# Optimization experiments

Measured on AMD Instinct MI355X. Metric: run time of the kernel, lower is better.

## Reference

```python
import jax, jax.numpy as jnp
import numpy as np

B, L, H, D, VOC, C, P = 16, 256, 6, 768, 32000, 20, 1
d = D // H
MAXF = 20
BN_EPS = 1e-5


def setup_inputs() -> dict:
    key = jax.random.key(0)
    ks = jax.random.split(key, 8)
    doc_tids = jax.random.randint(ks[0], (B, L), 0, VOC)
    TFs = jax.random.uniform(ks[1], (B, L), dtype=jnp.float32) * 20.0 + 1.0
    DFs = jax.random.uniform(ks[2], (B, L), dtype=jnp.float32) * 1000.0 + 1.0
    emb = jax.random.normal(ks[3], (VOC, D), dtype=jnp.float32) * 0.02
    fcW = jax.random.normal(ks[4], (C + P, D), dtype=jnp.float32) * 0.02
    fcb = jnp.zeros((C + P,), dtype=jnp.float32)
    weiW = jax.random.normal(ks[5], (2, H), dtype=jnp.float32) * 0.1
    weib = jnp.zeros((2,), dtype=jnp.float32)
    return dict(doc_tids=doc_tids, TFs=TFs, DFs=DFs, emb=emb,
                fcW=fcW, fcb=fcb, weiW=weiW, weib=weib)


def _bn(x):
    # BatchNorm over channel axis 1 (H), batch stats over all other axes (train mode, affine=False)
    m = x.mean(axis=(0, 2, 3), keepdims=True)
    v = x.var(axis=(0, 2, 3), keepdims=True)
    return (x - m) * jax.lax.rsqrt(v + BN_EPS)


def _leaky9(x):
    return jnp.where(x >= 0, x, 9.0 * x)


def reference(doc_tids, TFs, DFs, emb, fcW, fcb, weiW, weib):
    # --- EmbbedingTFIDF (eval mode, dropout off): tf-idf weighted embedding lookup ---
    tf = jnp.minimum(TFs, float(MAXF))
    idf = jnp.log1p(1.0 / DFs)
    x = emb[doc_tids] * (tf * idf)[:, :, None]          # (B, L, D)
    valid = doc_tids != 0
    # model flips pad_mask with logical_not, then co_weights[pad_mask] = 0
    invalid = ~(valid[:, :, None] & valid[:, None, :])  # (B, L, L) True -> zero out
    mask = invalid[:, None, :, :]                       # broadcast over heads

    def split_heads(h):
        return h.reshape(B, L, H, d).transpose(0, 2, 1, 3)  # (B, H, L, d)

    Q = split_heads(x)
    K = Q
    V = Q

    # --- nearAttention (layers=1) ---
    Vn = _bn(V)
    # DistMatrix: pairwise Euclidean distance dist[b,h,i,j] = ||K_i - Q_j||
    Ksq = jnp.sum(K * K, axis=-1)[..., :, None]
    Qsq = jnp.sum(Q * Q, axis=-1)[..., None, :]
    cross = jnp.einsum('bhid,bhjd->bhij', K, Q)
    co = jnp.sqrt(jnp.maximum(Ksq + Qsq - 2.0 * cross, 1e-12))  # (B, H, L, L)
    # BatchNorm1d(H) over flattened (B, H, L*L) == per-H stats over (0,2,3)
    co = _leaky9(_bn(co))
    co = jnp.where(mask, 0.0, co)
    co = jax.nn.softmax(co, axis=-1)
    co = jnp.where(jnp.isnan(co), 0.0, co)
    V_out = jnp.einsum('bhij,bhjd->bhid', co, Vn)
    Q_out = _bn(jnp.einsum('bhij,bhjd->bhid', co, Q))
    K_out = _bn(jnp.einsum('bhij,bhjd->bhid', co, K))

    # --- head ---
    Vc = V_out.transpose(0, 2, 1, 3).reshape(B, L, D)       # catHiddens
    V_lgts = jax.nn.softmax(Vc @ fcW.T + fcb, axis=-1)      # (B, L, C+P)
    cw = jnp.swapaxes(co, -1, -2).reshape(B, L * L, H)      # transpose then contiguous reshape
    cw = jax.nn.softmax(cw @ weiW.T + weib, axis=-1)        # (B, L*L, 2)
    cw = cw.reshape(B, L, L, 2).sum(axis=-2, keepdims=True)[:, :, :, 0]  # (B, L, 1)
    cw = jax.nn.softmax(cw, axis=-1)                        # softmax over singleton -> ones (faithful)
    logits = (cw * V_lgts).sum(axis=1)[:, :C]               # (B, C)
    logits = jax.nn.softmax(logits, axis=-1)
    return logits
```

## Files before the change

### kernel.cpp

```cpp
#include <hip/hip_runtime.h>
#include <hip/hip_bf16.h>
#include <math.h>

#define OFF_XH   0UL
#define OFF_XT   1572864UL
#define OFF_VC   3145728UL
#define OFF_SQ   4718592UL
#define OFF_PART 4767744UL
#define OFF_ACC  4780056UL
#define OFF_CTR  4780392UL
#define OFF_FCWB 4780396UL

typedef __attribute__((ext_vector_type(8))) __bf16 bf16x8;
typedef __attribute__((ext_vector_type(4))) float f32x4;
typedef __attribute__((ext_vector_type(8))) unsigned short u16x8;

__global__ __launch_bounds__(512) void k12_fused(const int* __restrict__ tids,
    const float* __restrict__ TF, const float* __restrict__ DF,
    const float* __restrict__ emb, unsigned short* __restrict__ xh,
    unsigned short* __restrict__ xT, float* __restrict__ sq,
    float* __restrict__ part, const float* __restrict__ fcW,
    unsigned short* __restrict__ fcWb, float* __restrict__ acc,
    unsigned int* __restrict__ ctr) {
  int bid = blockIdx.x;
  int xcd = bid & 7, idx = bid >> 3;
  int bh = xcd * 12 + idx % 12;
  int jq = idx / 12;
  int b = bh / 6, h = bh % 6;
  int tid = threadIdx.x;
  __shared__ unsigned short tile[32768];
  __shared__ float swd1[8], swd2[8], swv1[8], swv2[8];
  if (jq == 1) {
    if (tid < 168) {
      int i2 = bh * 168 + tid;
      fcWb[i2] = __bfloat16_as_ushort(__float2bfloat16(fcW[i2]));
    }
  } else if (jq == 0 && bh == 0) {
    if (tid < 336) acc[tid] = 0.0f;
    if (tid == 336) *ctr = 0u;
  }
  int sub = tid & 7, row0 = tid >> 3;
  int c16 = sub * 16;
  float ts1 = 0.0f, ts2 = 0.0f;
#pragma unroll
  for (int p = 0; p < 4; ++p) {
    int r = p * 64 + row0;
    int tok = b * 256 + r;
    int tv = tids[tok];
    float wgt = fminf(TF[tok], 20.0f) * log1pf(1.0f / DF[tok]);
    const float* er = emb + (size_t)tv * 768 + h * 128 + c16;
    float4 e0 = *(const float4*)er;
    float4 e1 = *(const float4*)(er + 4);
    float4 e2 = *(const float4*)(er + 8);
    float4 e3 = *(const float4*)(er + 12);
    float f[16] = {e0.x, e0.y, e0.z, e0.w, e1.x, e1.y, e1.z, e1.w,
                   e2.x, e2.y, e2.z, e2.w, e3.x, e3.y, e3.z, e3.w};
    u16x8 pk0, pk1;
    float s1 = 0.0f, s2 = 0.0f;
#pragma unroll
    for (int e = 0; e < 8; ++e) {
      __hip_bfloat16 hb = __float2bfloat16(f[e] * wgt);
      float g = __bfloat162float(hb);
      s1 += g; s2 += g * g;
      pk0[e] = __bfloat16_as_ushort(hb);
    }
#pragma unroll
    for (int e = 0; e < 8; ++e) {
      __hip_bfloat16 hb = __float2bfloat16(f[8 + e] * wgt);
      float g = __bfloat162float(hb);
      s1 += g; s2 += g * g;
      pk1[e] = __bfloat16_as_ushort(hb);
    }
    ts1 += s1; ts2 += s2;
    int rx = r & 7;
    *(u16x8*)&tile[r * 128 + (((sub * 2    ) ^ rx) * 8)] = pk0;
    *(u16x8*)&tile[r * 128 + (((sub * 2 + 1) ^ rx) * 8)] = pk1;
    if (jq == 0) {
      unsigned short* xo = xh + ((size_t)bh * 256 + r) * 128 + c16;
      *(u16x8*)xo = pk0;
      *(u16x8*)(xo + 8) = pk1;
    }
    s2 += __shfl_down(s2, 4); s2 += __shfl_down(s2, 2); s2 += __shfl_down(s2, 1);
    if (sub == 0)
      sq[(size_t)bh * 256 + r] = s2;
  }
  __syncthreads();
  if (jq == 3) {
    int ch = tid & 127, q = tid >> 7;
    int cc = ch >> 3, cs = ch & 7;
    unsigned int* xo = (unsigned int*)xT + ((size_t)bh * 128 + ch) * 128 + q * 32;
#pragma unroll
    for (int g = 0; g < 8; ++g) {
      unsigned int tmp[4];
#pragma unroll
      for (int k = 0; k < 4; ++k) {
        int t0 = q * 64 + (g * 4 + k) * 2;
        unsigned int lo = tile[ t0      * 128 + ((cc ^ ( t0      & 7)) * 8) + cs];
        unsigned int hi = tile[(t0 + 1) * 128 + ((cc ^ ((t0 + 1) & 7)) * 8) + cs];
        tmp[k] = lo | (hi << 16);
      }
      uint4 vv; vv.x = tmp[0]; vv.y = tmp[1]; vv.z = tmp[2]; vv.w = tmp[3];
      *(uint4*)(xo + g * 4) = vv;
    }
  }
  int w = tid >> 6, lane = tid & 63, quad = lane >> 4, l16 = lane & 15;
  const float* sqh = sq + (size_t)bh * 256;
  int it0 = w * 2;
  bf16x8 a2[2][4];
  float si2[2][4];
#pragma unroll
  for (int ith = 0; ith < 2; ++ith) {
    int ar = (it0 + ith) * 16 + l16, arx = ar & 7;
#pragma unroll
    for (int k0 = 0; k0 < 4; ++k0)
      a2[ith][k0] = *(const bf16x8*)&tile[ar * 128 + (((k0 * 4 + quad) ^ arx) * 8)];
#pragma unroll
    for (int r = 0; r < 4; ++r)
      si2[ith][r] = sqh[(it0 + ith) * 16 + quad * 4 + r];
  }
  float ls1 = 0.0f, ls2 = 0.0f;
#pragma unroll
  for (int jt = 0; jt < 4; ++jt) {
    int jr = jq * 64 + jt * 16 + l16, jrx = jr & 7;
    bf16x8 bfr[4];
#pragma unroll
    for (int k0 = 0; k0 < 4; ++k0)
      bfr[k0] = *(const bf16x8*)&tile[jr * 128 + (((k0 * 4 + quad) ^ jrx) * 8)];
    f32x4 acc0 = {0.0f, 0.0f, 0.0f, 0.0f}, acc1 = {0.0f, 0.0f, 0.0f, 0.0f};
#pragma unroll
    for (int k0 = 0; k0 < 4; ++k0) {
      acc0 = __builtin_amdgcn_mfma_f32_16x16x32_bf16(a2[0][k0], bfr[k0], acc0, 0, 0, 0);
      acc1 = __builtin_amdgcn_mfma_f32_16x16x32_bf16(a2[1][k0], bfr[k0], acc1, 0, 0, 0);
    }
    float sj = sqh[jr];
#pragma unroll
    for (int r = 0; r < 4; ++r) {
      float cv0 = sqrtf(fmaxf(si2[0][r] + sj - 2.0f * acc0[r], 1e-12f));
      float cv1 = sqrtf(fmaxf(si2[1][r] + sj - 2.0f * acc1[r], 1e-12f));
      ls1 += cv0 + cv1;
      ls2 += cv0 * cv0 + cv1 * cv1;
    }
  }
#pragma unroll
  for (int off = 32; off >= 1; off >>= 1) {
    ls1 += __shfl_down(ls1, off);
    ls2 += __shfl_down(ls2, off);
    ts1 += __shfl_down(ts1, off);
    ts2 += __shfl_down(ts2, off);
  }
  if (lane == 0) { swd1[w] = ls1; swd2[w] = ls2; swv1[w] = ts1; swv2[w] = ts2; }
  __syncthreads();
  if (tid == 0) {
    float d1 = 0.0f, d2 = 0.0f, v1 = 0.0f, v2 = 0.0f;
#pragma unroll
    for (int i = 0; i < 8; ++i) { d1 += swd1[i]; d2 += swd2[i]; v1 += swv1[i]; v2 += swv2[i]; }
    part[192 + (bh * 4 + jq) * 2 + 0] = d1;
    part[192 + (bh * 4 + jq) * 2 + 1] = d2;
    if (jq == 0) { part[bh * 2] = v1; part[bh * 2 + 1] = v2; }
  }
}

__global__ __launch_bounds__(256, 4) void k45_fused(const unsigned short* __restrict__ xh,
    const unsigned short* __restrict__ xT, const int* __restrict__ tids,
    const float* __restrict__ sq, const float* __restrict__ part,
    unsigned short* __restrict__ vc16) {
  int bid = blockIdx.x;
  int xcd = bid & 7, idx = bid >> 3;
  int bh = xcd * 12 + idx % 12;
  int p = idx / 12;
  int b = bh / 6, h = bh % 6;
  int tid = threadIdx.x, w = tid >> 6, lane = tid & 63;
  int quad = lane >> 4, l16 = lane & 15;
  int I = p * 16;
  __shared__ float svld[256];
  __shared__ float ssq[256];
  __shared__ unsigned short cot[16][264];
  __shared__ float smax[16][4];
  __shared__ float ssum[16][4];
  __shared__ float sstat[4];
  svld[tid] = (tids[b * 256 + tid] != 0) ? 1.0f : 0.0f;
  ssq[tid] = sq[(size_t)bh * 256 + tid];
  if (w == 0) {
    float c1 = 0.0f, c2 = 0.0f;
    {
      int bb = lane >> 2, jj = lane & 3;
      c1 = part[192 + ((bb * 6 + h) * 4 + jj) * 2 + 0];
      c2 = part[192 + ((bb * 6 + h) * 4 + jj) * 2 + 1];
    }
#pragma unroll
    for (int off = 32; off >= 1; off >>= 1) {
      c1 += __shfl_down(c1, off);
      c2 += __shfl_down(c2, off);
    }
    float v1 = 0.0f, v2 = 0.0f;
    if (lane < 16) {
      v1 = part[(lane * 6 + h) * 2 + 0];
      v2 = part[(lane * 6 + h) * 2 + 1];
    }
#pragma unroll
    for (int off = 8; off >= 1; off >>= 1) {
      v1 += __shfl_down(v1, off);
      v2 += __shfl_down(v2, off);
    }
    if (lane == 0) {
      float mean = c1 / 1048576.0f;
      float var = c2 / 1048576.0f - mean * mean;
      sstat[0] = mean;
      sstat[1] = rsqrtf(var + 1e-5f);
      float mv = v1 / 524288.0f;
      float vv = v2 / 524288.0f - mv * mv;
      sstat[2] = mv;
      sstat[3] = rsqrtf(vv + 1e-5f);
    }
  }
  const __bf16* xb = (const __bf16*)xh + (size_t)bh * 256 * 128;
  bf16x8 a[4];
#pragma unroll
  for (int k0 = 0; k0 < 4; ++k0)
    a[k0] = *(const bf16x8*)(xb + (size_t)(I + l16) * 128 + k0 * 32 + quad * 8);
  __syncthreads();
  float m = sstat[0], rsc = sstat[1];
  float rv[4], si[4];
#pragma unroll
  for (int r = 0; r < 4; ++r) {
    rv[r] = svld[I + quad * 4 + r];
    si[r] = ssq[I + quad * 4 + r];
  }
  float y[4][4];
#pragma unroll
  for (int tl = 0; tl < 4; ++tl) {
    int t = w * 4 + tl;
    f32x4 acc = {0.0f, 0.0f, 0.0f, 0.0f};
#pragma unroll
    for (int k0 = 0; k0 < 4; ++k0) {
      bf16x8 bfr = *(const bf16x8*)(xb + (size_t)(t * 16 + l16) * 128 + k0 * 32 + quad * 8);
      acc = __builtin_amdgcn_mfma_f32_16x16x32_bf16(a[k0], bfr, acc, 0, 0, 0);
    }
    float sj = ssq[t * 16 + l16];
    float cvld = svld[t * 16 + l16];
#pragma unroll
    for (int r = 0; r < 4; ++r) {
      float cv = sqrtf(fmaxf(si[r] + sj - 2.0f * acc[r], 1e-12f));
      float yv = (cv - m) * rsc;
      yv = yv >= 0.0f ? yv : 9.0f * yv;
      y[tl][r] = yv * rv[r] * cvld;
    }
  }
#pragma unroll
  for (int r = 0; r < 4; ++r) {
    float mx = fmaxf(fmaxf(y[0][r], y[1][r]), fmaxf(y[2][r], y[3][r]));
#pragma unroll
    for (int off = 1; off <= 8; off <<= 1) mx = fmaxf(mx, __shfl_xor(mx, off));
    if (l16 == 0) smax[quad * 4 + r][w] = mx;
  }
  __syncthreads();
  float gmx[4];
#pragma unroll
  for (int r = 0; r < 4; ++r) {
    int row = quad * 4 + r;
    gmx[r] = fmaxf(fmaxf(smax[row][0], smax[row][1]), fmaxf(smax[row][2], smax[row][3]));
    float s = 0.0f;
#pragma unroll
    for (int tl = 0; tl < 4; ++tl) { y[tl][r] = expf(y[tl][r] - gmx[r]); s += y[tl][r]; }
#pragma unroll
    for (int off = 1; off <= 8; off <<= 1) s += __shfl_xor(s, off);
    if (l16 == 0) ssum[row][w] = s;
  }
  __syncthreads();
#pragma unroll
  for (int r = 0; r < 4; ++r) {
    int row = quad * 4 + r;
    float gs = ssum[row][0] + ssum[row][1] + ssum[row][2] + ssum[row][3];
    float inv = 1.0f / gs;
#pragma unroll
    for (int tl = 0; tl < 4; ++tl)
      cot[row][w * 64 + tl * 16 + l16] =
          __bfloat16_as_ushort(__float2bfloat16(y[tl][r] * inv));
  }
  __syncthreads();
  bf16x8 a2[8];
#pragma unroll
  for (int k0 = 0; k0 < 8; ++k0)
    a2[k0] = *(const bf16x8*)&cot[l16][k0 * 32 + quad * 8];
  const __bf16* xbT = (const __bf16*)xT + (size_t)bh * 128 * 256;
  float mv = sstat[2], rvs = sstat[3];
  float rm = rvs * mv;
  size_t vbase = ((size_t)(b * 256 + I + quad * 4)) * 768 + h * 128;
#pragma unroll
  for (int jl = 0; jl < 2; ++jl) {
    int ch = (w * 2 + jl) * 16 + l16;
    const __bf16* brow = xbT + (size_t)ch * 256;
    f32x4 vacc = {0.0f, 0.0f, 0.0f, 0.0f};
#pragma unroll
    for (int k0 = 0; k0 < 8; ++k0) {
      bf16x8 bfr = *(const bf16x8*)(brow + k0 * 32 + quad * 8);
      vacc = __builtin_amdgcn_mfma_f32_16x16x32_bf16(a2[k0], bfr, vacc, 0, 0, 0);
    }
#pragma unroll
    for (int r = 0; r < 4; ++r) {
      float ov = rvs * vacc[r] - rm;
      vc16[vbase + (size_t)r * 768 + ch] = __bfloat16_as_ushort(__float2bfloat16(ov));
    }
  }
}

__global__ __launch_bounds__(256) void k5b6_lgts(const unsigned short* __restrict__ vc16,
    const unsigned short* __restrict__ fcWb, const float* __restrict__ fcb,
    float* __restrict__ acc, unsigned int* __restrict__ ctr, float* __restrict__ out) {
  int bid = blockIdx.x;
  int xcd = bid & 7, idx = bid >> 3;
  int b = xcd * 2 + (idx & 1);
  int qa = idx >> 1;
  int tid = threadIdx.x, w = tid >> 6, lane = tid & 63;
  int quad = lane >> 4, l16 = lane & 15;
  int tok0 = b * 256 + qa * 64 + w * 16;
  int c1c = (l16 < 5) ? (16 + l16) : 20;
  const __bf16* vb = (const __bf16*)vc16;
  const __bf16* w0 = (const __bf16*)fcWb + (size_t)l16 * 768;
  const __bf16* w1 = (const __bf16*)fcWb + (size_t)c1c * 768;
  f32x4 ac0 = {0.0f, 0.0f, 0.0f, 0.0f}, ac1 = {0.0f, 0.0f, 0.0f, 0.0f};
#pragma unroll
  for (int k0 = 0; k0 < 24; ++k0) {
    int ko = k0 * 32 + quad * 8;
    bf16x8 af = *(const bf16x8*)(vb + (size_t)(tok0 + l16) * 768 + ko);
    bf16x8 b0 = *(const bf16x8*)(w0 + ko);
    bf16x8 b1 = *(const bf16x8*)(w1 + ko);
    ac0 = __builtin_amdgcn_mfma_f32_16x16x32_bf16(af, b0, ac0, 0, 0, 0);
    ac1 = __builtin_amdgcn_mfma_f32_16x16x32_bf16(af, b1, ac1, 0, 0, 0);
  }
  float bias0 = fcb[l16];
  float bias1 = (l16 < 5) ? fcb[16 + l16] : 0.0f;
  float p0s = 0.0f, p1s = 0.0f;
#pragma unroll
  for (int r = 0; r < 4; ++r) {
    float lg0 = ac0[r] + bias0;
    float lg1 = (l16 < 5) ? (ac1[r] + bias1) : -1e30f;
    float mx = fmaxf(lg0, lg1);
#pragma unroll
    for (int off = 1; off <= 8; off <<= 1) mx = fmaxf(mx, __shfl_xor(mx, off));
    float e0 = expf(lg0 - mx), e1 = expf(lg1 - mx);
    float s = e0 + e1;
#pragma unroll
    for (int off = 1; off <= 8; off <<= 1) s += __shfl_xor(s, off);
    float inv = 1.0f / s;
    p0s += e0 * inv;
    p1s += e1 * inv;
  }
  p0s += __shfl_xor(p0s, 16); p0s += __shfl_xor(p0s, 32);
  p1s += __shfl_xor(p1s, 16); p1s += __shfl_xor(p1s, 32);
  __shared__ float sacc[4][21];
  __shared__ unsigned int sdone;
  if (quad == 0) sacc[w][l16] = p0s;
  if (quad == 1 && l16 < 5) sacc[w][16 + l16] = p1s;
  __syncthreads();
  if (tid < 21) {
    float s = sacc[0][tid] + sacc[1][tid] + sacc[2][tid] + sacc[3][tid];
    atomicAdd(&acc[b * 21 + tid], s);
  }
  __syncthreads();
  if (tid == 0) {
    __threadfence();
    sdone = atomicAdd(ctr, 1u);
  }
  __syncthreads();
  if (sdone == 63u && tid < 16) {
    float v[20];
    float mx = -1e30f;
#pragma unroll
    for (int c = 0; c < 20; ++c) {
      v[c] = atomicAdd(&acc[tid * 21 + c], 0.0f);
      mx = fmaxf(mx, v[c]);
    }
    float s = 0.0f;
#pragma unroll
    for (int c = 0; c < 20; ++c) { v[c] = expf(v[c] - mx); s += v[c]; }
    float inv = 1.0f / s;
#pragma unroll
    for (int c = 0; c < 20; ++c) out[tid * 20 + c] = v[c] * inv;
  }
}

extern "C" void kernel_launch(void* const* d_in, const int* in_sizes, int n_in,
                              void* d_out, int out_size, void* d_ws, size_t ws_size,
                              hipStream_t stream) {
  const int*   tids = (const int*)d_in[0];
  const float* TF   = (const float*)d_in[1];
  const float* DF   = (const float*)d_in[2];
  const float* emb  = (const float*)d_in[3];
  const float* fcW  = (const float*)d_in[4];
  const float* fcb  = (const float*)d_in[5];
  float* out = (float*)d_out;
  float* ws  = (float*)d_ws;
  unsigned short* xh   = (unsigned short*)(ws + OFF_XH);
  unsigned short* xT   = (unsigned short*)(ws + OFF_XT);
  unsigned short* vc   = (unsigned short*)(ws + OFF_VC);
  unsigned short* fcWb = (unsigned short*)(ws + OFF_FCWB);
  float* sq    = ws + OFF_SQ;
  float* part  = ws + OFF_PART;
  float* acc   = ws + OFF_ACC;
  unsigned int* ctr = (unsigned int*)(ws + OFF_CTR);

  k12_fused<<<384, 512, 0, stream>>>(tids, TF, DF, emb, xh, xT, sq, part,
                                     fcW, fcWb, acc, ctr);
  k45_fused<<<1536, 256, 0, stream>>>(xh, xT, tids, sq, part, vc);
  k5b6_lgts<<<64, 256, 0, stream>>>(vc, fcWb, fcb, acc, ctr, out);
}
```

Measured before the change: 191.8 us.

## Store distance matrix in first kernel and reload it instead of recomputing

The first kernel now writes each pairwise distance value to a new fp32 workspace region while computing BN statistics. The second kernel loads its 16-row slice of that matrix into shared memory rather than recomputing the K·Q MFMA products, squared norms and sqrt. This trades MFMA and sqrt work for about 25 MB of global writes plus the matching reads. The stats reduction loops are also merged into a single shuffle loop.

```diff
diff --git a/kernel.cpp b/kernel.cpp
--- a/kernel.cpp
+++ b/kernel.cpp
@@ -10,6 +10,7 @@
 #define OFF_ACC  4780056UL
 #define OFF_CTR  4780392UL
 #define OFF_FCWB 4780396UL
+#define OFF_CV   8388608UL
 
 typedef __attribute__((ext_vector_type(8))) __bf16 bf16x8;
 typedef __attribute__((ext_vector_type(4))) float f32x4;
@@ -21,7 +22,7 @@
     unsigned short* __restrict__ xT, float* __restrict__ sq,
     float* __restrict__ part, const float* __restrict__ fcW,
     unsigned short* __restrict__ fcWb, float* __restrict__ acc,
-    unsigned int* __restrict__ ctr) {
+    unsigned int* __restrict__ ctr, float* __restrict__ cvws) {
   int bid = blockIdx.x;
   int xcd = bid & 7, idx = bid >> 3;
   int bh = xcd * 12 + idx % 12;
@@ -121,22 +122,25 @@
   float ls1 = 0.0f, ls2 = 0.0f;
 #pragma unroll
   for (int jt = 0; jt < 4; ++jt) {
-    int jr = jq * 64 + jt * 16 + l16, jrx = jr & 7;
+    int jcol = jq * 64 + jt * 16 + l16;
+    int jrx = jcol & 7;
     bf16x8 bfr[4];
 #pragma unroll
     for (int k0 = 0; k0 < 4; ++k0)
-      bfr[k0] = *(const bf16x8*)&tile[jr * 128 + (((k0 * 4 + quad) ^ jrx) * 8)];
+      bfr[k0] = *(const bf16x8*)&tile[jcol * 128 + (((k0 * 4 + quad) ^ jrx) * 8)];
     f32x4 acc0 = {0.0f, 0.0f, 0.0f, 0.0f}, acc1 = {0.0f, 0.0f, 0.0f, 0.0f};
 #pragma unroll
     for (int k0 = 0; k0 < 4; ++k0) {
       acc0 = __builtin_amdgcn_mfma_f32_16x16x32_bf16(a2[0][k0], bfr[k0], acc0, 0, 0, 0);
       acc1 = __builtin_amdgcn_mfma_f32_16x16x32_bf16(a2[1][k0], bfr[k0], acc1, 0, 0, 0);
     }
-    float sj = sqh[jr];
+    float sj = sqh[jcol];
 #pragma unroll
     for (int r = 0; r < 4; ++r) {
       float cv0 = sqrtf(fmaxf(si2[0][r] + sj - 2.0f * acc0[r], 1e-12f));
       float cv1 = sqrtf(fmaxf(si2[1][r] + sj - 2.0f * acc1[r], 1e-12f));
+      cvws[((size_t)bh * 256 + (it0    ) * 16 + quad * 4 + r) * 256 + jcol] = cv0;
+      cvws[((size_t)bh * 256 + (it0 + 1) * 16 + quad * 4 + r) * 256 + jcol] = cv1;
       ls1 += cv0 + cv1;
       ls2 += cv0 * cv0 + cv1 * cv1;
     }
@@ -160,10 +164,9 @@
   }
 }
 
-__global__ __launch_bounds__(256, 4) void k45_fused(const unsigned short* __restrict__ xh,
+__global__ __launch_bounds__(256, 4) void k45_fused(const float* __restrict__ cvws,
     const unsigned short* __restrict__ xT, const int* __restrict__ tids,
-    const float* __restrict__ sq, const float* __restrict__ part,
-    unsigned short* __restrict__ vc16) {
+    const float* __restrict__ part, unsigned short* __restrict__ vc16) {
   int bid = blockIdx.x;
   int xcd = bid & 7, idx = bid >> 3;
   int bh = xcd * 12 + idx % 12;
@@ -172,14 +175,25 @@
   int tid = threadIdx.x, w = tid >> 6, lane = tid & 63;
   int quad = lane >> 4, l16 = lane & 15;
   int I = p * 16;
+  __shared__ float scv[16][257];
   __shared__ float svld[256];
-  __shared__ float ssq[256];
   __shared__ unsigned short cot[16][264];
   __shared__ float smax[16][4];
   __shared__ float ssum[16][4];
   __shared__ float sstat[4];
   svld[tid] = (tids[b * 256 + tid] != 0) ? 1.0f : 0.0f;
-  ssq[tid] = sq[(size_t)bh * 256 + tid];
+  {
+    int row = tid >> 4, cseg = (tid & 15) * 16;
+    const float* src = cvws + ((size_t)bh * 256 + I + row) * 256 + cseg;
+    float4 v0 = *(const float4*)src;
+    float4 v1 = *(const float4*)(src + 4);
+    float4 v2 = *(const float4*)(src + 8);
+    float4 v3 = *(const float4*)(src + 12);
+    *(float4*)&scv[row][cseg + 0]  = v0;
+    *(float4*)&scv[row][cseg + 4]  = v1;
+    *(float4*)&scv[row][cseg + 8]  = v2;
+    *(float4*)&scv[row][cseg + 12] = v3;
+  }
   if (w == 0) {
     float c1 = 0.0f, c2 = 0.0f;
     {
@@ -187,18 +201,15 @@
       c1 = part[192 + ((bb * 6 + h) * 4 + jj) * 2 + 0];
       c2 = part[192 + ((bb * 6 + h) * 4 + jj) * 2 + 1];
     }
-#pragma unroll
-    for (int off = 32; off >= 1; off >>= 1) {
-      c1 += __shfl_down(c1, off);
-      c2 += __shfl_down(c2, off);
-    }
     float v1 = 0.0f, v2 = 0.0f;
     if (lane < 16) {
       v1 = part[(lane * 6 + h) * 2 + 0];
       v2 = part[(lane * 6 + h) * 2 + 1];
     }
 #pragma unroll
-    for (int off = 8; off >= 1; off >>= 1) {
+    for (int off = 32; off >= 1; off >>= 1) {
+      c1 += __shfl_down(c1, off);
+      c2 += __shfl_down(c2, off);
       v1 += __shfl_down(v1, off);
       v2 += __shfl_down(v2, off);
     }
@@ -213,34 +224,19 @@
       sstat[3] = rsqrtf(vv + 1e-5f);
     }
   }
-  const __bf16* xb = (const __bf16*)xh + (size_t)bh * 256 * 128;
-  bf16x8 a[4];
-#pragma unroll
-  for (int k0 = 0; k0 < 4; ++k0)
-    a[k0] = *(const bf16x8*)(xb + (size_t)(I + l16) * 128 + k0 * 32 + quad * 8);
   __syncthreads();
   float m = sstat[0], rsc = sstat[1];
-  float rv[4], si[4];
-#pragma unroll
-  for (int r = 0; r < 4; ++r) {
-    rv[r] = svld[I + quad * 4 + r];
-    si[r] = ssq[I + quad * 4 + r];
-  }
+  float rv[4];
+#pragma unroll
+  for (int r = 0; r < 4; ++r) rv[r] = svld[I + quad * 4 + r];
   float y[4][4];
 #pragma unroll
   for (int tl = 0; tl < 4; ++tl) {
     int t = w * 4 + tl;
-    f32x4 acc = {0.0f, 0.0f, 0.0f, 0.0f};
-#pragma unroll
-    for (int k0 = 0; k0 < 4; ++k0) {
-      bf16x8 bfr = *(const bf16x8*)(xb + (size_t)(t * 16 + l16) * 128 + k0 * 32 + quad * 8);
-      acc = __builtin_amdgcn_mfma_f32_16x16x32_bf16(a[k0], bfr, acc, 0, 0, 0);
-    }
-    float sj = ssq[t * 16 + l16];
     float cvld = svld[t * 16 + l16];
 #pragma unroll
     for (int r = 0; r < 4; ++r) {
-      float cv = sqrtf(fmaxf(si[r] + sj - 2.0f * acc[r], 1e-12f));
+      float cv = scv[quad * 4 + r][t * 16 + l16];
       float yv = (cv - m) * rsc;
       yv = yv >= 0.0f ? yv : 9.0f * yv;
       y[tl][r] = yv * rv[r] * cvld;
@@ -398,10 +394,11 @@
   float* sq    = ws + OFF_SQ;
   float* part  = ws + OFF_PART;
   float* acc   = ws + OFF_ACC;
+  float* cvws  = ws + OFF_CV;
   unsigned int* ctr = (unsigned int*)(ws + OFF_CTR);
 
   k12_fused<<<384, 512, 0, stream>>>(tids, TF, DF, emb, xh, xT, sq, part,
-                                     fcW, fcWb, acc, ctr);
-  k45_fused<<<1536, 256, 0, stream>>>(xh, xT, tids, sq, part, vc);
+                                     fcW, fcWb, acc, ctr, cvws);
+  k45_fused<<<1536, 256, 0, stream>>>(cvws, xT, tids, part, vc);
   k5b6_lgts<<<64, 256, 0, stream>>>(vc, fcWb, fcb, acc, ctr, out);
 }
```

Measured after the change: 188.0 us. No clear change (-2.0%).
